# Performance work log

Hardware: AMD Instinct MI355X
Metric: run time of the kernel (lower is better)

The kernel has to match this reference:

```python
import jax, jax.numpy as jnp
import numpy as np

N_NODES = 100000

def gcn_conv(x, W, b, src, dst, deg_isqrt):
    # x: [N, Fin] -> lin -> [N, Fout]; aggregate src->dst with sym norm; + bias
    h = x @ W                                   # [N, Fout]
    norm = deg_isqrt[src] * deg_isqrt[dst]      # [E+N]
    msg = h[src] * norm[:, None]                # [E+N, Fout]
    out = jax.ops.segment_sum(msg, dst, num_segments=N_NODES)
    return out + b

def setup_inputs() -> dict:
    key = jax.random.key(0)
    k1, k2, k3, k4 = jax.random.split(key, 4)
    x = jax.random.normal(k1, (N_NODES, 256), dtype=jnp.float32)
    edge_index = jax.random.randint(k2, (2, 3200000), 0, N_NODES, dtype=jnp.int32)
    # Glorot-ish params for GCNConv(256->16) and GCNConv(16->1)
    W1 = jax.random.normal(k3, (256, 16), dtype=jnp.float32) * (1.0 / np.sqrt(256))
    b1 = jnp.zeros((16,), dtype=jnp.float32)
    W2 = jax.random.normal(k4, (16, 1), dtype=jnp.float32) * (1.0 / np.sqrt(16))
    b2 = jnp.zeros((1,), dtype=jnp.float32)
    return {"x": x, "edge_index": edge_index, "W1": W1, "b1": b1, "W2": W2, "b2": b2}

def reference(x, edge_index, W1, b1, W2, b2):
    # GCNConv adds self-loops then symmetric normalization deg^{-1/2}
    loops = jnp.arange(N_NODES, dtype=edge_index.dtype)
    src = jnp.concatenate([edge_index[0], loops])
    dst = jnp.concatenate([edge_index[1], loops])
    deg = jax.ops.segment_sum(jnp.ones_like(src, dtype=x.dtype), dst, num_segments=N_NODES)
    deg_isqrt = jnp.where(deg > 0, jax.lax.rsqrt(deg), 0.0)

    h = gcn_conv(x, W1, b1, src, dst, deg_isqrt)
    h = jax.nn.relu(h)
    # dropout(p=0.5, train=self.training): eval mode -> identity (deterministic reference)
    out = gcn_conv(h, W2, b2, src, dst, deg_isqrt)
    return out  # [N, 1]
```

## Files before the change

kernel.cpp:

```cpp
#include <hip/hip_runtime.h>
#include <hip/hip_fp16.h>


#define SBSH 8
#define SBCAP 10240
#define LCAP 9216
#define HPAD 400
#define GSTR 16
#define PEDG 8192

__global__ void k_init(int* __restrict__ gcur, int Bsb) {
    int i = blockIdx.x * blockDim.x + threadIdx.x;
    if (i < Bsb) gcur[i * GSTR] = i * SBCAP;
}

__global__ __launch_bounds__(1024) void k_p1(
    const int* __restrict__ src, const int* __restrict__ dst,
    int* __restrict__ gcur, int* __restrict__ pairs, int E, int Bsb)
{
    __shared__ int s2[PEDG];
    __shared__ unsigned short rid[PEDG];
    __shared__ int hist[392];
    __shared__ int loc[392];
    __shared__ int gbase[392];
    __shared__ int wsum[8];
    const int t = threadIdx.x;
    const int base4 = blockIdx.x * (PEDG / 4);
    for (int i = t; i < 392; i += 1024) hist[i] = 0;
    __syncthreads();

    int4 dd[2], ss[2], rk[2];
    #pragma unroll
    for (int r = 0; r < 2; ++r) {
        const int i4 = base4 + r * 1024 + t;
        const int i = i4 << 2;
        int4 v, s;
        if (i + 3 < E) {
            v = ((const int4*)dst)[i4];
            s = ((const int4*)src)[i4];
        } else {
            v.x = (i     < E) ? dst[i]     : -1;
            v.y = (i + 1 < E) ? dst[i + 1] : -1;
            v.z = (i + 2 < E) ? dst[i + 2] : -1;
            v.w = (i + 3 < E) ? dst[i + 3] : -1;
            s.x = (i     < E) ? src[i]     : 0;
            s.y = (i + 1 < E) ? src[i + 1] : 0;
            s.z = (i + 2 < E) ? src[i + 2] : 0;
            s.w = (i + 3 < E) ? src[i + 3] : 0;
        }
        dd[r] = v; ss[r] = s;
        int4 q = make_int4(0, 0, 0, 0);
        if (v.x >= 0) q.x = atomicAdd(&hist[v.x >> SBSH], 1);
        if (v.y >= 0) q.y = atomicAdd(&hist[v.y >> SBSH], 1);
        if (v.z >= 0) q.z = atomicAdd(&hist[v.z >> SBSH], 1);
        if (v.w >= 0) q.w = atomicAdd(&hist[v.w >> SBSH], 1);
        rk[r] = q;
    }
    __syncthreads();
    int c = 0, vv = 0;
    if (t < 391) {
        const int lane = t & 63, w = t >> 6;
        c = hist[t];
        vv = c;
        #pragma unroll
        for (int off = 1; off < 64; off <<= 1) {
            int u = __shfl_up(vv, off, 64);
            if (lane >= off) vv += u;
        }
        if (lane == 63 || t == 390) wsum[w] = vv;
    }
    __syncthreads();
    if (t < 391) {
        const int w = t >> 6;
        int add = 0;
        #pragma unroll
        for (int i = 0; i < 6; ++i) if (i < w) add += wsum[i];
        int inc = vv + add, exc = inc - c;
        loc[t] = exc;
        if (t == 390) loc[391] = inc;
        gbase[t] = c ? atomicAdd(&gcur[t * GSTR], c) : 0;
    }
    __syncthreads();
    const int tot = loc[391];
    #pragma unroll
    for (int r = 0; r < 2; ++r) {
        int4 v = dd[r], s = ss[r], q = rk[r];
        if (v.x >= 0) { int sb = v.x >> SBSH; int p = loc[sb] + q.x; s2[p] = (s.x << SBSH) | (v.x & 255); rid[p] = (unsigned short)sb; }
        if (v.y >= 0) { int sb = v.y >> SBSH; int p = loc[sb] + q.y; s2[p] = (s.y << SBSH) | (v.y & 255); rid[p] = (unsigned short)sb; }
        if (v.z >= 0) { int sb = v.z >> SBSH; int p = loc[sb] + q.z; s2[p] = (s.z << SBSH) | (v.z & 255); rid[p] = (unsigned short)sb; }
        if (v.w >= 0) { int sb = v.w >> SBSH; int p = loc[sb] + q.w; s2[p] = (s.w << SBSH) | (v.w & 255); rid[p] = (unsigned short)sb; }
    }
    __syncthreads();
    for (int i = t; i < tot; i += 1024) {
        const int sb = rid[i];
        pairs[gbase[sb] + (i - loc[sb])] = s2[i];
    }
}

__global__ __launch_bounds__(1024) void k_sortsb(
    int* __restrict__ pairs, const int* __restrict__ gcur,
    int* __restrict__ rowp, float* __restrict__ isq, int N)
{
    __shared__ int s2[LCAP];
    __shared__ int hist[256];
    __shared__ int exc[256];
    __shared__ int wsum[4];
    const int t = threadIdx.x, sb = blockIdx.x;
    const int beg = sb * SBCAP;
    int cnt = gcur[sb * GSTR] - beg;
    if (cnt > LCAP) cnt = LCAP;
    if (t < 256) hist[t] = 0;
    __syncthreads();
    const int c4 = cnt >> 2;
    const int4* p4 = (const int4*)(pairs + beg);
    int4 va[3], ra[3];
    int vr = 0, rr = 0;
    #pragma unroll
    for (int k = 0; k < 3; ++k) {
        const int i = t + k * 1024;
        if (i < c4) {
            int4 v = p4[i];
            va[k] = v;
            ra[k].x = atomicAdd(&hist[v.x & 255], 1);
            ra[k].y = atomicAdd(&hist[v.y & 255], 1);
            ra[k].z = atomicAdd(&hist[v.z & 255], 1);
            ra[k].w = atomicAdd(&hist[v.w & 255], 1);
        }
    }
    {
        const int i = (c4 << 2) + t;
        if (i < cnt) { vr = pairs[beg + i]; rr = atomicAdd(&hist[vr & 255], 1); }
    }
    __syncthreads();
    int c = 0, v = 0;
    if (t < 256) {
        const int lane = t & 63, w = t >> 6;
        c = hist[t];
        v = c;
        #pragma unroll
        for (int off = 1; off < 64; off <<= 1) {
            int u = __shfl_up(v, off, 64);
            if (lane >= off) v += u;
        }
        if (lane == 63) wsum[w] = v;
    }
    __syncthreads();
    if (t < 256) {
        const int w = t >> 6;
        int add = 0;
        #pragma unroll
        for (int i = 0; i < 3; ++i) if (i < w) add += wsum[i];
        int inc = v + add;
        int e0 = inc - c;
        exc[t] = e0;
        rowp[sb * 257 + t] = e0;
        if (t == 255) rowp[sb * 257 + 256] = inc;
        int n = (sb << SBSH) + t;
        if (n < N) isq[n] = rsqrtf((float)(c + 1));
    }
    __syncthreads();
    #pragma unroll
    for (int k = 0; k < 3; ++k) {
        const int i = t + k * 1024;
        if (i < c4) {
            int4 v2 = va[k], q = ra[k];
            s2[exc[v2.x & 255] + q.x] = v2.x >> SBSH;
            s2[exc[v2.y & 255] + q.y] = v2.y >> SBSH;
            s2[exc[v2.z & 255] + q.z] = v2.z >> SBSH;
            s2[exc[v2.w & 255] + q.w] = v2.w >> SBSH;
        }
    }
    {
        const int i = (c4 << 2) + t;
        if (i < cnt) s2[exc[vr & 255] + rr] = vr >> SBSH;
    }
    __syncthreads();
    {
        int4* pw = (int4*)(pairs + beg);
        const int4* s4 = (const int4*)s2;
        for (int i = t; i < c4; i += 1024) pw[i] = s4[i];
        for (int i = (c4 << 2) + t; i < cnt; i += 1024) pairs[beg + i] = s2[i];
    }
}

__global__ __launch_bounds__(256) void k_lin1(
    const float* __restrict__ x, const float* __restrict__ W1,
    const float* __restrict__ isq, __half* __restrict__ hs16, int N)
{
    __shared__ float part[128][16];
    const int t = threadIdx.x;
    const int w = t >> 6, lane = t & 63;
    const int hu = __builtin_amdgcn_readfirstlane(w >> 1);
    const int nl = ((w & 1) << 6) + lane;
    const int n = blockIdx.x * 128 + nl;
    const int nc = (n < N) ? n : (N - 1);
    const float4* xr = (const float4*)(x + ((size_t)nc << 8) + (hu << 7));
    float acc[16];
    #pragma unroll
    for (int f = 0; f < 16; ++f) acc[f] = 0.f;
    #pragma unroll 1
    for (int kb = 0; kb < 4; ++kb) {
        float4 xa[8];
        #pragma unroll
        for (int u = 0; u < 8; ++u) xa[u] = xr[(kb << 3) + u];
        #pragma unroll
        for (int u = 0; u < 8; ++u) {
            const int k4 = (kb << 3) + u;
            const float4* wr = (const float4*)W1 + (hu << 9) + (k4 << 4);
            const float xv[4] = { xa[u].x, xa[u].y, xa[u].z, xa[u].w };
            #pragma unroll
            for (int j = 0; j < 4; ++j) {
                #pragma unroll
                for (int f4 = 0; f4 < 4; ++f4) {
                    const float4 wv = wr[(j << 2) + f4];
                    acc[(f4 << 2) + 0] = fmaf(xv[j], wv.x, acc[(f4 << 2) + 0]);
                    acc[(f4 << 2) + 1] = fmaf(xv[j], wv.y, acc[(f4 << 2) + 1]);
                    acc[(f4 << 2) + 2] = fmaf(xv[j], wv.z, acc[(f4 << 2) + 2]);
                    acc[(f4 << 2) + 3] = fmaf(xv[j], wv.w, acc[(f4 << 2) + 3]);
                }
            }
        }
    }
    if (hu == 1) {
        #pragma unroll
        for (int f4 = 0; f4 < 4; ++f4) {
            const int fs = (f4 ^ (nl & 3)) << 2;
            *(float4*)&part[nl][fs] =
                make_float4(acc[(f4 << 2) + 0], acc[(f4 << 2) + 1],
                            acc[(f4 << 2) + 2], acc[(f4 << 2) + 3]);
        }
    }
    __syncthreads();
    if (hu == 0 && n < N) {
        #pragma unroll
        for (int f4 = 0; f4 < 4; ++f4) {
            const int fs = (f4 ^ (nl & 3)) << 2;
            float4 p = *(const float4*)&part[nl][fs];
            acc[(f4 << 2) + 0] += p.x;
            acc[(f4 << 2) + 1] += p.y;
            acc[(f4 << 2) + 2] += p.z;
            acc[(f4 << 2) + 3] += p.w;
        }
        const float iq = isq[n];
        __half2* o = (__half2*)&hs16[(size_t)n << 4];
        #pragma unroll
        for (int f2 = 0; f2 < 8; ++f2)
            o[f2] = __floats2half2_rn(acc[2 * f2] * iq, acc[2 * f2 + 1] * iq);
    }
}

__global__ __launch_bounds__(256) void k_agg1(
    const int* __restrict__ sorted, const int* __restrict__ rowp,
    const __half* __restrict__ hs16, const float* __restrict__ isq,
    const float* __restrict__ b1, const float* __restrict__ W2,
    float* __restrict__ ts, int N)
{
    const int t = threadIdx.x, g = blockIdx.x;
    const int l = t >> 3, q = t & 3, p = (t >> 2) & 1;
    const int n = g * 32 + l;
    if (n >= N) return;
    const int sb = n >> SBSH, L = n & 255;
    const int rbeg = sb * SBCAP + rowp[sb * 257 + L];
    const int rend = sb * SBCAP + rowp[sb * 257 + L + 1];
    const float2* h2 = (const float2*)hs16;
    float a0 = 0.f, a1 = 0.f, a2 = 0.f, a3 = 0.f;
    for (int j = rbeg + p; j < rend; j += 2) {
        int s0 = sorted[j];
        float2 ra = h2[s0 * 4 + q];
        union { float f; __half2 h; } ca0, ca1;
        ca0.f = ra.x; ca1.f = ra.y;
        float2 fa0 = __half22float2(ca0.h), fa1 = __half22float2(ca1.h);
        a0 += fa0.x; a1 += fa0.y; a2 += fa1.x; a3 += fa1.y;
    }
    a0 += __shfl_xor(a0, 4);
    a1 += __shfl_xor(a1, 4);
    a2 += __shfl_xor(a2, 4);
    a3 += __shfl_xor(a3, 4);
    {
        float2 rs = h2[(size_t)n * 4 + q];
        union { float f; __half2 h; } c0, c1;
        c0.f = rs.x; c1.f = rs.y;
        float2 f0 = __half22float2(c0.h), f1 = __half22float2(c1.h);
        a0 += f0.x; a1 += f0.y; a2 += f1.x; a3 += f1.y;
    }
    const float iq = isq[n];
    const int f0i = q * 4;
    float pr = fmaxf(a0 * iq + b1[f0i + 0], 0.f) * W2[f0i + 0]
             + fmaxf(a1 * iq + b1[f0i + 1], 0.f) * W2[f0i + 1]
             + fmaxf(a2 * iq + b1[f0i + 2], 0.f) * W2[f0i + 2]
             + fmaxf(a3 * iq + b1[f0i + 3], 0.f) * W2[f0i + 3];
    pr += __shfl_xor(pr, 1);
    pr += __shfl_xor(pr, 2);
    if ((t & 7) == 0) ts[n] = pr * iq;
}

__global__ __launch_bounds__(256) void k_agg2(
    const int* __restrict__ sorted, const int* __restrict__ rowp,
    const float* __restrict__ ts, const float* __restrict__ isq,
    const float* __restrict__ b2, float* __restrict__ out, int N)
{
    const int t = threadIdx.x;
    const int l = t >> 3, q = t & 7;
    const int n = blockIdx.x * 32 + l;
    if (n >= N) return;
    const int sb = n >> SBSH, L = n & 255;
    const int rbeg = sb * SBCAP + rowp[sb * 257 + L];
    const int rend = sb * SBCAP + rowp[sb * 257 + L + 1];
    float acc = 0.f;
    for (int j = rbeg + q; j < rend; j += 8) acc += ts[sorted[j]];
    acc += __shfl_xor(acc, 1);
    acc += __shfl_xor(acc, 2);
    acc += __shfl_xor(acc, 4);
    if (q == 0) out[n] = (acc + ts[n]) * isq[n] + b2[0];
}

extern "C" void kernel_launch(void* const* d_in, const int* in_sizes, int n_in,
                              void* d_out, int out_size, void* d_ws, size_t ws_size,
                              hipStream_t stream) {
    const float* x  = (const float*)d_in[0];
    const int*   ei = (const int*)d_in[1];
    const float* W1 = (const float*)d_in[2];
    const float* b1 = (const float*)d_in[3];
    const float* W2 = (const float*)d_in[4];
    const float* b2 = (const float*)d_in[5];
    const int N = in_sizes[0] / 256;
    const int E = in_sizes[1] / 2;
    const int* src = ei;
    const int* dst = ei + E;
    const int Bsb = (N + 255) >> SBSH;

    char* w = (char*)d_ws;
    float*  isq   = (float*)w;  w += (size_t)N * 4;
    int*    gcur  = (int*)w;    w += (size_t)HPAD * GSTR * 4;
    int*    pairs = (int*)w;    w += (size_t)Bsb * SBCAP * 4;
    int*    rowp  = (int*)w;    w += (size_t)Bsb * 257 * 4;
    __half* hs16  = (__half*)w; w += (size_t)N * 32;
    float*  ts    = (float*)w;  w += (size_t)N * 4;
    float*  out   = (float*)d_out;

    k_init<<<(Bsb + 255) / 256, 256, 0, stream>>>(gcur, Bsb);

    const int nbBin = (E + PEDG - 1) / PEDG;
    k_p1<<<nbBin, 1024, 0, stream>>>(src, dst, gcur, pairs, E, Bsb);

    k_sortsb<<<Bsb, 1024, 0, stream>>>(pairs, gcur, rowp, isq, N);

    k_lin1<<<(N + 127) / 128, 256, 0, stream>>>(x, W1, isq, hs16, N);

    k_agg1<<<(N + 31) / 32, 256, 0, stream>>>(pairs, rowp, hs16, isq, b1, W2, ts, N);
    k_agg2<<<(N + 31) / 32, 256, 0, stream>>>(pairs, rowp, ts, isq, b2, out, N);
}
```

Before: 260.8 us.

## Co-schedule edge binning and dense projection in one heterogeneous kernel

Merges the edge-binning pass and the x@W1 projection into one launch. Some blocks bin edges and the rest compute the linear layer, so the memory-bound x read overlaps with the scatter work. Because the projection now runs before degrees are known, the source-side degree scaling moves into aggregation as a per-edge isq[src] gather with FMA. This adds one random 4-byte load per edge. Bin blocks shrink to 512 threads and PEDG halves to fit the shared-memory union.

Result: slower. 286.5 us (+9.8%).

```diff
diff --git a/kernel.cpp b/kernel.cpp
--- a/kernel.cpp
+++ b/kernel.cpp
@@ -7,93 +7,162 @@
 #define LCAP 9216
 #define HPAD 400
 #define GSTR 16
-#define PEDG 8192
+#define PEDG 4096
 
 __global__ void k_init(int* __restrict__ gcur, int Bsb) {
     int i = blockIdx.x * blockDim.x + threadIdx.x;
     if (i < Bsb) gcur[i * GSTR] = i * SBCAP;
 }
 
-__global__ __launch_bounds__(1024) void k_p1(
+__global__ __launch_bounds__(512, 8) void k_mix(
     const int* __restrict__ src, const int* __restrict__ dst,
-    int* __restrict__ gcur, int* __restrict__ pairs, int E, int Bsb)
+    int* __restrict__ gcur, int* __restrict__ pairs, int E, int Bsb, int nbBin,
+    const float* __restrict__ x, const float* __restrict__ W1,
+    __half* __restrict__ hs16, int N)
 {
-    __shared__ int s2[PEDG];
-    __shared__ unsigned short rid[PEDG];
-    __shared__ int hist[392];
-    __shared__ int loc[392];
-    __shared__ int gbase[392];
-    __shared__ int wsum[8];
+    __shared__ union {
+        struct {
+            int s2[PEDG];
+            unsigned short rid[PEDG];
+            int hist[392], loc[392], gbase[392];
+            int wsum[8];
+        } p;
+        struct { float part[2][128][16]; } l;
+    } U;
     const int t = threadIdx.x;
-    const int base4 = blockIdx.x * (PEDG / 4);
-    for (int i = t; i < 392; i += 1024) hist[i] = 0;
-    __syncthreads();
-
-    int4 dd[2], ss[2], rk[2];
-    #pragma unroll
-    for (int r = 0; r < 2; ++r) {
-        const int i4 = base4 + r * 1024 + t;
-        const int i = i4 << 2;
-        int4 v, s;
-        if (i + 3 < E) {
-            v = ((const int4*)dst)[i4];
-            s = ((const int4*)src)[i4];
-        } else {
-            v.x = (i     < E) ? dst[i]     : -1;
-            v.y = (i + 1 < E) ? dst[i + 1] : -1;
-            v.z = (i + 2 < E) ? dst[i + 2] : -1;
-            v.w = (i + 3 < E) ? dst[i + 3] : -1;
-            s.x = (i     < E) ? src[i]     : 0;
-            s.y = (i + 1 < E) ? src[i + 1] : 0;
-            s.z = (i + 2 < E) ? src[i + 2] : 0;
-            s.w = (i + 3 < E) ? src[i + 3] : 0;
-        }
-        dd[r] = v; ss[r] = s;
-        int4 q = make_int4(0, 0, 0, 0);
-        if (v.x >= 0) q.x = atomicAdd(&hist[v.x >> SBSH], 1);
-        if (v.y >= 0) q.y = atomicAdd(&hist[v.y >> SBSH], 1);
-        if (v.z >= 0) q.z = atomicAdd(&hist[v.z >> SBSH], 1);
-        if (v.w >= 0) q.w = atomicAdd(&hist[v.w >> SBSH], 1);
-        rk[r] = q;
-    }
-    __syncthreads();
-    int c = 0, vv = 0;
-    if (t < 391) {
-        const int lane = t & 63, w = t >> 6;
-        c = hist[t];
-        vv = c;
-        #pragma unroll
-        for (int off = 1; off < 64; off <<= 1) {
-            int u = __shfl_up(vv, off, 64);
-            if (lane >= off) vv += u;
-        }
-        if (lane == 63 || t == 390) wsum[w] = vv;
-    }
-    __syncthreads();
-    if (t < 391) {
-        const int w = t >> 6;
-        int add = 0;
-        #pragma unroll
-        for (int i = 0; i < 6; ++i) if (i < w) add += wsum[i];
-        int inc = vv + add, exc = inc - c;
-        loc[t] = exc;
-        if (t == 390) loc[391] = inc;
-        gbase[t] = c ? atomicAdd(&gcur[t * GSTR], c) : 0;
-    }
-    __syncthreads();
-    const int tot = loc[391];
-    #pragma unroll
-    for (int r = 0; r < 2; ++r) {
-        int4 v = dd[r], s = ss[r], q = rk[r];
-        if (v.x >= 0) { int sb = v.x >> SBSH; int p = loc[sb] + q.x; s2[p] = (s.x << SBSH) | (v.x & 255); rid[p] = (unsigned short)sb; }
-        if (v.y >= 0) { int sb = v.y >> SBSH; int p = loc[sb] + q.y; s2[p] = (s.y << SBSH) | (v.y & 255); rid[p] = (unsigned short)sb; }
-        if (v.z >= 0) { int sb = v.z >> SBSH; int p = loc[sb] + q.z; s2[p] = (s.z << SBSH) | (v.z & 255); rid[p] = (unsigned short)sb; }
-        if (v.w >= 0) { int sb = v.w >> SBSH; int p = loc[sb] + q.w; s2[p] = (s.w << SBSH) | (v.w & 255); rid[p] = (unsigned short)sb; }
-    }
-    __syncthreads();
-    for (int i = t; i < tot; i += 1024) {
-        const int sb = rid[i];
-        pairs[gbase[sb] + (i - loc[sb])] = s2[i];
+
+    if (blockIdx.x < (unsigned)nbBin) {
+        const int base4 = blockIdx.x * (PEDG / 4);
+        for (int i = t; i < 392; i += 512) U.p.hist[i] = 0;
+        __syncthreads();
+
+        int4 dd[2], ss[2], rk[2];
+        #pragma unroll
+        for (int r = 0; r < 2; ++r) {
+            const int i4 = base4 + r * 512 + t;
+            const int i = i4 << 2;
+            int4 v, s;
+            if (i + 3 < E) {
+                v = ((const int4*)dst)[i4];
+                s = ((const int4*)src)[i4];
+            } else {
+                v.x = (i     < E) ? dst[i]     : -1;
+                v.y = (i + 1 < E) ? dst[i + 1] : -1;
+                v.z = (i + 2 < E) ? dst[i + 2] : -1;
+                v.w = (i + 3 < E) ? dst[i + 3] : -1;
+                s.x = (i     < E) ? src[i]     : 0;
+                s.y = (i + 1 < E) ? src[i + 1] : 0;
+                s.z = (i + 2 < E) ? src[i + 2] : 0;
+                s.w = (i + 3 < E) ? src[i + 3] : 0;
+            }
+            dd[r] = v; ss[r] = s;
+            int4 q = make_int4(0, 0, 0, 0);
+            if (v.x >= 0) q.x = atomicAdd(&U.p.hist[v.x >> SBSH], 1);
+            if (v.y >= 0) q.y = atomicAdd(&U.p.hist[v.y >> SBSH], 1);
+            if (v.z >= 0) q.z = atomicAdd(&U.p.hist[v.z >> SBSH], 1);
+            if (v.w >= 0) q.w = atomicAdd(&U.p.hist[v.w >> SBSH], 1);
+            rk[r] = q;
+        }
+        __syncthreads();
+        int c = 0, vv = 0;
+        if (t < 391) {
+            const int lane = t & 63, w = t >> 6;
+            c = U.p.hist[t];
+            vv = c;
+            #pragma unroll
+            for (int off = 1; off < 64; off <<= 1) {
+                int u = __shfl_up(vv, off, 64);
+                if (lane >= off) vv += u;
+            }
+            if (lane == 63 || t == 390) U.p.wsum[w] = vv;
+        }
+        __syncthreads();
+        if (t < 391) {
+            const int w = t >> 6;
+            int add = 0;
+            #pragma unroll
+            for (int i = 0; i < 6; ++i) if (i < w) add += U.p.wsum[i];
+            int inc = vv + add, exc = inc - c;
+            U.p.loc[t] = exc;
+            if (t == 390) U.p.loc[391] = inc;
+            U.p.gbase[t] = c ? atomicAdd(&gcur[t * GSTR], c) : 0;
+        }
+        __syncthreads();
+        const int tot = U.p.loc[391];
+        #pragma unroll
+        for (int r = 0; r < 2; ++r) {
+            int4 v = dd[r], s = ss[r], q = rk[r];
+            if (v.x >= 0) { int sb = v.x >> SBSH; int p = U.p.loc[sb] + q.x; U.p.s2[p] = (s.x << SBSH) | (v.x & 255); U.p.rid[p] = (unsigned short)sb; }
+            if (v.y >= 0) { int sb = v.y >> SBSH; int p = U.p.loc[sb] + q.y; U.p.s2[p] = (s.y << SBSH) | (v.y & 255); U.p.rid[p] = (unsigned short)sb; }
+            if (v.z >= 0) { int sb = v.z >> SBSH; int p = U.p.loc[sb] + q.z; U.p.s2[p] = (s.z << SBSH) | (v.z & 255); U.p.rid[p] = (unsigned short)sb; }
+            if (v.w >= 0) { int sb = v.w >> SBSH; int p = U.p.loc[sb] + q.w; U.p.s2[p] = (s.w << SBSH) | (v.w & 255); U.p.rid[p] = (unsigned short)sb; }
+        }
+        __syncthreads();
+        for (int i = t; i < tot; i += 512) {
+            const int sb = U.p.rid[i];
+            pairs[U.p.gbase[sb] + (i - U.p.loc[sb])] = U.p.s2[i];
+        }
+    } else {
+        const int b2 = blockIdx.x - nbBin;
+        const int grp = t >> 8;
+        const int w2 = (t >> 6) & 3;
+        const int lane = t & 63;
+        const int hu = __builtin_amdgcn_readfirstlane(w2 >> 1);
+        const int nl = ((w2 & 1) << 6) + lane;
+        const int n = b2 * 256 + grp * 128 + nl;
+        const int nc = (n < N) ? n : (N - 1);
+        const float4* xr = (const float4*)(x + ((size_t)nc << 8) + (hu << 7));
+        float acc[16];
+        #pragma unroll
+        for (int f = 0; f < 16; ++f) acc[f] = 0.f;
+        #pragma unroll 1
+        for (int kb = 0; kb < 8; ++kb) {
+            float4 xa[4];
+            #pragma unroll
+            for (int u = 0; u < 4; ++u) xa[u] = xr[(kb << 2) + u];
+            #pragma unroll
+            for (int u = 0; u < 4; ++u) {
+                const int k4 = (kb << 2) + u;
+                const float4* wr = (const float4*)W1 + (hu << 9) + (k4 << 4);
+                const float xv[4] = { xa[u].x, xa[u].y, xa[u].z, xa[u].w };
+                #pragma unroll
+                for (int j = 0; j < 4; ++j) {
+                    #pragma unroll
+                    for (int f4 = 0; f4 < 4; ++f4) {
+                        const float4 wv = wr[(j << 2) + f4];
+                        acc[(f4 << 2) + 0] = fmaf(xv[j], wv.x, acc[(f4 << 2) + 0]);
+                        acc[(f4 << 2) + 1] = fmaf(xv[j], wv.y, acc[(f4 << 2) + 1]);
+                        acc[(f4 << 2) + 2] = fmaf(xv[j], wv.z, acc[(f4 << 2) + 2]);
+                        acc[(f4 << 2) + 3] = fmaf(xv[j], wv.w, acc[(f4 << 2) + 3]);
+                    }
+                }
+            }
+        }
+        if (hu == 1) {
+            #pragma unroll
+            for (int f4 = 0; f4 < 4; ++f4) {
+                const int fs = (f4 ^ (nl & 3)) << 2;
+                *(float4*)&U.l.part[grp][nl][fs] =
+                    make_float4(acc[(f4 << 2) + 0], acc[(f4 << 2) + 1],
+                                acc[(f4 << 2) + 2], acc[(f4 << 2) + 3]);
+            }
+        }
+        __syncthreads();
+        if (hu == 0 && n < N) {
+            #pragma unroll
+            for (int f4 = 0; f4 < 4; ++f4) {
+                const int fs = (f4 ^ (nl & 3)) << 2;
+                float4 p = *(const float4*)&U.l.part[grp][nl][fs];
+                acc[(f4 << 2) + 0] += p.x;
+                acc[(f4 << 2) + 1] += p.y;
+                acc[(f4 << 2) + 2] += p.z;
+                acc[(f4 << 2) + 3] += p.w;
+            }
+            __half2* o = (__half2*)&hs16[(size_t)n << 4];
+            #pragma unroll
+            for (int f2 = 0; f2 < 8; ++f2)
+                o[f2] = __floats2half2_rn(acc[2 * f2], acc[2 * f2 + 1]);
+        }
     }
 }
 
@@ -180,72 +249,6 @@
         const int4* s4 = (const int4*)s2;
         for (int i = t; i < c4; i += 1024) pw[i] = s4[i];
         for (int i = (c4 << 2) + t; i < cnt; i += 1024) pairs[beg + i] = s2[i];
-    }
-}
-
-__global__ __launch_bounds__(256) void k_lin1(
-    const float* __restrict__ x, const float* __restrict__ W1,
-    const float* __restrict__ isq, __half* __restrict__ hs16, int N)
-{
-    __shared__ float part[128][16];
-    const int t = threadIdx.x;
-    const int w = t >> 6, lane = t & 63;
-    const int hu = __builtin_amdgcn_readfirstlane(w >> 1);
-    const int nl = ((w & 1) << 6) + lane;
-    const int n = blockIdx.x * 128 + nl;
-    const int nc = (n < N) ? n : (N - 1);
-    const float4* xr = (const float4*)(x + ((size_t)nc << 8) + (hu << 7));
-    float acc[16];
-    #pragma unroll
-    for (int f = 0; f < 16; ++f) acc[f] = 0.f;
-    #pragma unroll 1
-    for (int kb = 0; kb < 4; ++kb) {
-        float4 xa[8];
-        #pragma unroll
-        for (int u = 0; u < 8; ++u) xa[u] = xr[(kb << 3) + u];
-        #pragma unroll
-        for (int u = 0; u < 8; ++u) {
-            const int k4 = (kb << 3) + u;
-            const float4* wr = (const float4*)W1 + (hu << 9) + (k4 << 4);
-            const float xv[4] = { xa[u].x, xa[u].y, xa[u].z, xa[u].w };
-            #pragma unroll
-            for (int j = 0; j < 4; ++j) {
-                #pragma unroll
-                for (int f4 = 0; f4 < 4; ++f4) {
-                    const float4 wv = wr[(j << 2) + f4];
-                    acc[(f4 << 2) + 0] = fmaf(xv[j], wv.x, acc[(f4 << 2) + 0]);
-                    acc[(f4 << 2) + 1] = fmaf(xv[j], wv.y, acc[(f4 << 2) + 1]);
-                    acc[(f4 << 2) + 2] = fmaf(xv[j], wv.z, acc[(f4 << 2) + 2]);
-                    acc[(f4 << 2) + 3] = fmaf(xv[j], wv.w, acc[(f4 << 2) + 3]);
-                }
-            }
-        }
-    }
-    if (hu == 1) {
-        #pragma unroll
-        for (int f4 = 0; f4 < 4; ++f4) {
-            const int fs = (f4 ^ (nl & 3)) << 2;
-            *(float4*)&part[nl][fs] =
-                make_float4(acc[(f4 << 2) + 0], acc[(f4 << 2) + 1],
-                            acc[(f4 << 2) + 2], acc[(f4 << 2) + 3]);
-        }
-    }
-    __syncthreads();
-    if (hu == 0 && n < N) {
-        #pragma unroll
-        for (int f4 = 0; f4 < 4; ++f4) {
-            const int fs = (f4 ^ (nl & 3)) << 2;
-            float4 p = *(const float4*)&part[nl][fs];
-            acc[(f4 << 2) + 0] += p.x;
-            acc[(f4 << 2) + 1] += p.y;
-            acc[(f4 << 2) + 2] += p.z;
-            acc[(f4 << 2) + 3] += p.w;
-        }
-        const float iq = isq[n];
-        __half2* o = (__half2*)&hs16[(size_t)n << 4];
-        #pragma unroll
-        for (int f2 = 0; f2 < 8; ++f2)
-            o[f2] = __floats2half2_rn(acc[2 * f2] * iq, acc[2 * f2 + 1] * iq);
     }
 }
 
@@ -266,24 +269,27 @@
     float a0 = 0.f, a1 = 0.f, a2 = 0.f, a3 = 0.f;
     for (int j = rbeg + p; j < rend; j += 2) {
         int s0 = sorted[j];
+        float w = isq[s0];
         float2 ra = h2[s0 * 4 + q];
         union { float f; __half2 h; } ca0, ca1;
         ca0.f = ra.x; ca1.f = ra.y;
         float2 fa0 = __half22float2(ca0.h), fa1 = __half22float2(ca1.h);
-        a0 += fa0.x; a1 += fa0.y; a2 += fa1.x; a3 += fa1.y;
+        a0 = fmaf(fa0.x, w, a0); a1 = fmaf(fa0.y, w, a1);
+        a2 = fmaf(fa1.x, w, a2); a3 = fmaf(fa1.y, w, a3);
     }
     a0 += __shfl_xor(a0, 4);
     a1 += __shfl_xor(a1, 4);
     a2 += __shfl_xor(a2, 4);
     a3 += __shfl_xor(a3, 4);
+    const float iq = isq[n];
     {
         float2 rs = h2[(size_t)n * 4 + q];
         union { float f; __half2 h; } c0, c1;
         c0.f = rs.x; c1.f = rs.y;
         float2 f0 = __half22float2(c0.h), f1 = __half22float2(c1.h);
-        a0 += f0.x; a1 += f0.y; a2 += f1.x; a3 += f1.y;
-    }
-    const float iq = isq[n];
+        a0 = fmaf(f0.x, iq, a0); a1 = fmaf(f0.y, iq, a1);
+        a2 = fmaf(f1.x, iq, a2); a3 = fmaf(f1.y, iq, a3);
+    }
     const int f0i = q * 4;
     float pr = fmaxf(a0 * iq + b1[f0i + 0], 0.f) * W2[f0i + 0]
              + fmaxf(a1 * iq + b1[f0i + 1], 0.f) * W2[f0i + 1]
@@ -341,11 +347,11 @@
     k_init<<<(Bsb + 255) / 256, 256, 0, stream>>>(gcur, Bsb);
 
     const int nbBin = (E + PEDG - 1) / PEDG;
-    k_p1<<<nbBin, 1024, 0, stream>>>(src, dst, gcur, pairs, E, Bsb);
+    const int nLin  = (N + 255) / 256;
+    k_mix<<<nbBin + nLin, 512, 0, stream>>>(src, dst, gcur, pairs, E, Bsb,
+                                            nbBin, x, W1, hs16, N);
 
     k_sortsb<<<Bsb, 1024, 0, stream>>>(pairs, gcur, rowp, isq, N);
-
-    k_lin1<<<(N + 127) / 128, 256, 0, stream>>>(x, W1, isq, hs16, N);
 
     k_agg1<<<(N + 31) / 32, 256, 0, stream>>>(pairs, rowp, hs16, isq, b1, W2, ts, N);
     k_agg2<<<(N + 31) / 32, 256, 0, stream>>>(pairs, rowp, ts, isq, b2, out, N);
```

## Fuse per-superblock sort with first linear layer into one kernel

Applied to the files above, without the earlier changes.

Merges the per-superblock counting sort kernel and the x@W1 linear kernel into a single 1024-thread kernel per 256-node superblock. The linear work now splits K four ways across wave groups and reduces partials through shared memory that is unioned with the sort buffer, and it reuses the locally computed inverse-sqrt degrees. This removes one launch and the global round trip of isq, but it ties the memory-bound x read to the sort's grid of about 391 blocks and adds a serialized four-step shared-memory reduction with extra barriers.

Result: no change. 264.2 us (+1.3%).

```diff
diff --git a/kernel.cpp b/kernel.cpp
--- a/kernel.cpp
+++ b/kernel.cpp
@@ -97,14 +97,20 @@
     }
 }
 
-__global__ __launch_bounds__(1024) void k_sortsb(
+__global__ __launch_bounds__(1024) void k_sl(
     int* __restrict__ pairs, const int* __restrict__ gcur,
-    int* __restrict__ rowp, float* __restrict__ isq, int N)
+    int* __restrict__ rowp, float* __restrict__ isq,
+    const float* __restrict__ x, const float* __restrict__ W1,
+    __half* __restrict__ hs16, int N)
 {
-    __shared__ int s2[LCAP];
+    __shared__ union {
+        int s2[LCAP];
+        float part[256][16];
+    } U;
     __shared__ int hist[256];
     __shared__ int exc[256];
     __shared__ int wsum[4];
+    __shared__ float isql[256];
     const int t = threadIdx.x, sb = blockIdx.x;
     const int beg = sb * SBCAP;
     int cnt = gcur[sb * GSTR] - beg;
@@ -155,8 +161,10 @@
         exc[t] = e0;
         rowp[sb * 257 + t] = e0;
         if (t == 255) rowp[sb * 257 + 256] = inc;
-        int n = (sb << SBSH) + t;
-        if (n < N) isq[n] = rsqrtf((float)(c + 1));
+        const float iqv = rsqrtf((float)(c + 1));
+        isql[t] = iqv;
+        int n0 = (sb << SBSH) + t;
+        if (n0 < N) isq[n0] = iqv;
     }
     __syncthreads();
     #pragma unroll
@@ -164,49 +172,43 @@
         const int i = t + k * 1024;
         if (i < c4) {
             int4 v2 = va[k], q = ra[k];
-            s2[exc[v2.x & 255] + q.x] = v2.x >> SBSH;
-            s2[exc[v2.y & 255] + q.y] = v2.y >> SBSH;
-            s2[exc[v2.z & 255] + q.z] = v2.z >> SBSH;
-            s2[exc[v2.w & 255] + q.w] = v2.w >> SBSH;
+            U.s2[exc[v2.x & 255] + q.x] = v2.x >> SBSH;
+            U.s2[exc[v2.y & 255] + q.y] = v2.y >> SBSH;
+            U.s2[exc[v2.z & 255] + q.z] = v2.z >> SBSH;
+            U.s2[exc[v2.w & 255] + q.w] = v2.w >> SBSH;
         }
     }
     {
         const int i = (c4 << 2) + t;
-        if (i < cnt) s2[exc[vr & 255] + rr] = vr >> SBSH;
+        if (i < cnt) U.s2[exc[vr & 255] + rr] = vr >> SBSH;
     }
     __syncthreads();
     {
         int4* pw = (int4*)(pairs + beg);
-        const int4* s4 = (const int4*)s2;
+        const int4* s4 = (const int4*)U.s2;
         for (int i = t; i < c4; i += 1024) pw[i] = s4[i];
-        for (int i = (c4 << 2) + t; i < cnt; i += 1024) pairs[beg + i] = s2[i];
-    }
-}
-
-__global__ __launch_bounds__(256) void k_lin1(
-    const float* __restrict__ x, const float* __restrict__ W1,
-    const float* __restrict__ isq, __half* __restrict__ hs16, int N)
-{
-    __shared__ float part[128][16];
-    const int t = threadIdx.x;
+        for (int i = (c4 << 2) + t; i < cnt; i += 1024) pairs[beg + i] = U.s2[i];
+    }
+    __syncthreads();
+
     const int w = t >> 6, lane = t & 63;
-    const int hu = __builtin_amdgcn_readfirstlane(w >> 1);
-    const int nl = ((w & 1) << 6) + lane;
-    const int n = blockIdx.x * 128 + nl;
+    const int kq = __builtin_amdgcn_readfirstlane(w & 3);
+    const int nl = ((w >> 2) << 6) + lane;
+    const int n = (sb << SBSH) + nl;
     const int nc = (n < N) ? n : (N - 1);
-    const float4* xr = (const float4*)(x + ((size_t)nc << 8) + (hu << 7));
+    const float4* xr = (const float4*)(x + ((size_t)nc << 8) + (kq << 6));
     float acc[16];
     #pragma unroll
     for (int f = 0; f < 16; ++f) acc[f] = 0.f;
     #pragma unroll 1
     for (int kb = 0; kb < 4; ++kb) {
-        float4 xa[8];
-        #pragma unroll
-        for (int u = 0; u < 8; ++u) xa[u] = xr[(kb << 3) + u];
-        #pragma unroll
-        for (int u = 0; u < 8; ++u) {
-            const int k4 = (kb << 3) + u;
-            const float4* wr = (const float4*)W1 + (hu << 9) + (k4 << 4);
+        float4 xa[4];
+        #pragma unroll
+        for (int u = 0; u < 4; ++u) xa[u] = xr[(kb << 2) + u];
+        #pragma unroll
+        for (int u = 0; u < 4; ++u) {
+            const int k4 = (kb << 2) + u;
+            const float4* wr = (const float4*)W1 + (kq << 8) + (k4 << 4);
             const float xv[4] = { xa[u].x, xa[u].y, xa[u].z, xa[u].w };
             #pragma unroll
             for (int j = 0; j < 4; ++j) {
@@ -221,31 +223,38 @@
             }
         }
     }
-    if (hu == 1) {
-        #pragma unroll
-        for (int f4 = 0; f4 < 4; ++f4) {
-            const int fs = (f4 ^ (nl & 3)) << 2;
-            *(float4*)&part[nl][fs] =
-                make_float4(acc[(f4 << 2) + 0], acc[(f4 << 2) + 1],
-                            acc[(f4 << 2) + 2], acc[(f4 << 2) + 3]);
-        }
-    }
-    __syncthreads();
-    if (hu == 0 && n < N) {
-        #pragma unroll
-        for (int f4 = 0; f4 < 4; ++f4) {
-            const int fs = (f4 ^ (nl & 3)) << 2;
-            float4 p = *(const float4*)&part[nl][fs];
-            acc[(f4 << 2) + 0] += p.x;
-            acc[(f4 << 2) + 1] += p.y;
-            acc[(f4 << 2) + 2] += p.z;
-            acc[(f4 << 2) + 3] += p.w;
-        }
-        const float iq = isq[n];
-        __half2* o = (__half2*)&hs16[(size_t)n << 4];
-        #pragma unroll
-        for (int f2 = 0; f2 < 8; ++f2)
-            o[f2] = __floats2half2_rn(acc[2 * f2] * iq, acc[2 * f2 + 1] * iq);
+    #pragma unroll 1
+    for (int r = 0; r < 4; ++r) {
+        if (kq == r) {
+            #pragma unroll
+            for (int f4 = 0; f4 < 4; ++f4) {
+                const int fs = (f4 ^ (nl & 3)) << 2;
+                float4 vv = make_float4(acc[(f4 << 2) + 0], acc[(f4 << 2) + 1],
+                                        acc[(f4 << 2) + 2], acc[(f4 << 2) + 3]);
+                if (r == 0) {
+                    *(float4*)&U.part[nl][fs] = vv;
+                } else {
+                    float4 p = *(const float4*)&U.part[nl][fs];
+                    p.x += vv.x; p.y += vv.y; p.z += vv.z; p.w += vv.w;
+                    *(float4*)&U.part[nl][fs] = p;
+                }
+            }
+        }
+        __syncthreads();
+    }
+    if (t < 256) {
+        const int n2 = (sb << SBSH) + t;
+        if (n2 < N) {
+            const float iqv = isql[t];
+            __half2* o = (__half2*)&hs16[(size_t)n2 << 4];
+            #pragma unroll
+            for (int f4 = 0; f4 < 4; ++f4) {
+                const int fs = (f4 ^ (t & 3)) << 2;
+                float4 p = *(const float4*)&U.part[t][fs];
+                o[f4 * 2 + 0] = __floats2half2_rn(p.x * iqv, p.y * iqv);
+                o[f4 * 2 + 1] = __floats2half2_rn(p.z * iqv, p.w * iqv);
+            }
+        }
     }
 }
 
@@ -343,9 +352,7 @@
     const int nbBin = (E + PEDG - 1) / PEDG;
     k_p1<<<nbBin, 1024, 0, stream>>>(src, dst, gcur, pairs, E, Bsb);
 
-    k_sortsb<<<Bsb, 1024, 0, stream>>>(pairs, gcur, rowp, isq, N);
-
-    k_lin1<<<(N + 127) / 128, 256, 0, stream>>>(x, W1, isq, hs16, N);
+    k_sl<<<Bsb, 1024, 0, stream>>>(pairs, gcur, rowp, isq, x, W1, hs16, N);
 
     k_agg1<<<(N + 31) / 32, 256, 0, stream>>>(pairs, rowp, hs16, isq, b1, W2, ts, N);
     k_agg2<<<(N + 31) / 32, 256, 0, stream>>>(pairs, rowp, ts, isq, b2, out, N);
```
